# Performance work log

Measured on AMD Instinct MI355X. Metric: run time of the kernel, lower is better.

## Reference

```python
import jax, jax.numpy as jnp
import numpy as np

M, B, C = 8, 65536, 100  # model_num, batch_size, choice_size


def setup_inputs() -> dict:
    key = jax.random.key(0)
    k1, k2, k3, k4, k5, k6 = jax.random.split(key, 6)
    x = jax.random.normal(k1, (B, C), dtype=jnp.float32)
    z = jax.random.normal(k2, (M, B, C), dtype=jnp.float32)
    # choice index per customer; value == C means "no purchase" -> all-zero row
    choice = jax.random.randint(k3, (B,), 0, C + 1)
    y = (jnp.arange(C)[None, :] == choice[:, None]).astype(jnp.float32)
    alpha = jax.random.uniform(k4, (M,), dtype=jnp.float32)
    alpha = alpha / alpha.sum()  # mixture weights
    u_previous = jax.random.normal(k5, (M,), dtype=jnp.float32)
    u = jax.random.normal(k6, (), dtype=jnp.float32)
    return {"x": x, "y": y, "z": z, "alpha": alpha,
            "u_previous": u_previous, "u": u}


def reference(x, y, z, alpha, u_previous, u):
    u = jnp.reshape(u, ())
    has_y = jnp.sum(y, axis=-1) > 0                       # [B] purchased?
    # --- mixture term g (per customer), detached like torch's float(g) ---
    zy = jnp.einsum('mbc,bc->mb', z, y)                   # sum(z[j,i]*y[i])
    exp_up = jnp.exp(u_previous)[:, None]                 # [M,1]
    denom_z = exp_up + jnp.sum(jnp.exp(z), axis=-1)       # [M,B]
    num_z = jnp.where(has_y[None, :], jnp.exp(zy), exp_up)
    g = jnp.sum(alpha[:, None] * num_z / denom_z, axis=0)  # [B]
    g = jax.lax.stop_gradient(g)                          # float(g) in torch
    # --- outer model likelihood ratio ---
    xy = jnp.sum(x * y, axis=-1)                          # [B]
    denom_x = jnp.exp(u) + jnp.sum(jnp.exp(x), axis=-1)   # [B]
    num_x = jnp.where(has_y, jnp.exp(xy), jnp.exp(u))     # [B]
    loss = jnp.mean(num_x / (denom_x * g))
    return -loss
```

## Files before the change

### kernel.cpp

```cpp
#include <hip/hip_runtime.h>


constexpr int Mn = 8;
constexpr int Bn = 65536;
constexpr int Cn = 100;

__global__ __launch_bounds__(256, 4) void mmnl_kernel(
    const float* __restrict__ x,
    const float* __restrict__ y,
    const float* __restrict__ z,
    const float* __restrict__ alpha,
    const float* __restrict__ u_previous,
    const float* __restrict__ u_scalar,
    float* __restrict__ out)
{
    const int lane = threadIdx.x & 63;
    const int wib  = threadIdx.x >> 6;
    const int wid  = blockIdx.x * 4 + wib;
    const int nw   = gridDim.x * 4;

    const float exp_u = __expf(u_scalar[0]);
    float a_m[Mn], eup[Mn];
    #pragma unroll
    for (int m = 0; m < Mn; ++m) {
        a_m[m] = alpha[m];
        eup[m] = __expf(u_previous[m]);
    }

    const int  c0  = lane;
    const int  c1  = lane + 64;
    const bool hc1 = (c1 < Cn);

    float acc = 0.0f;

    for (int b = wid; b < Bn; b += nw) {
        const float* xb = x + (size_t)b * Cn;
        const float* yb = y + (size_t)b * Cn;
        float xv0 = xb[c0];
        float yv0 = yb[c0];
        float xv1 = hc1 ? xb[c1] : 0.0f;
        float yv1 = hc1 ? yb[c1] : 0.0f;

        float zv0[Mn], zv1[Mn];
        #pragma unroll
        for (int m = 0; m < Mn; ++m) {
            const float* zr = z + ((size_t)m * Bn + b) * (size_t)Cn;
            zv0[m] = zr[c0];
            zv1[m] = hc1 ? zr[c1] : 0.0f;
        }

        unsigned long long b0 = __ballot(yv0 > 0.5f);
        unsigned long long b1 = __ballot(yv1 > 0.5f);
        const bool has_y = (b0 | b1) != 0ULL;
        int  src  = 0;
        bool use1 = false;
        if (b0)       { src = __ffsll(b0) - 1; }
        else if (b1)  { src = __ffsll(b1) - 1; use1 = true; }

        float sex = __expf(xv0) + (hc1 ? __expf(xv1) : 0.0f);
        #pragma unroll
        for (int off = 32; off; off >>= 1)
            sex += __shfl_xor(sex, off, 64);

        float xy = __shfl(use1 ? xv1 : xv0, src, 64);

        float g = 0.0f;
        #pragma unroll
        for (int m = 0; m < Mn; ++m) {
            float sez = __expf(zv0[m]) + (hc1 ? __expf(zv1[m]) : 0.0f);
            #pragma unroll
            for (int off = 32; off; off >>= 1)
                sez += __shfl_xor(sez, off, 64);
            float zy  = __shfl(use1 ? zv1[m] : zv0[m], src, 64);
            float num = has_y ? __expf(zy) : eup[m];
            g += a_m[m] * num / (eup[m] + sez);
        }

        const float denom_x = exp_u + sex;
        const float num_x   = has_y ? __expf(xy) : exp_u;
        acc += num_x / (denom_x * g);
    }

    __shared__ float bsum[4];
    if (lane == 0) bsum[wib] = acc;
    __syncthreads();
    if (threadIdx.x == 0) {
        float s = (bsum[0] + bsum[1]) + (bsum[2] + bsum[3]);
        atomicAdd(out, -s * (1.0f / (float)Bn));
    }
}

extern "C" void kernel_launch(void* const* d_in, const int* in_sizes, int n_in,
                              void* d_out, int out_size, void* d_ws, size_t ws_size,
                              hipStream_t stream) {
    const float* x  = (const float*)d_in[0];
    const float* y  = (const float*)d_in[1];
    const float* z  = (const float*)d_in[2];
    const float* al = (const float*)d_in[3];
    const float* up = (const float*)d_in[4];
    const float* u  = (const float*)d_in[5];

    float* out = (float*)d_out;
    hipMemsetAsync(out, 0, sizeof(float), stream);

    dim3 grid(2048), block(256);
    mmnl_kernel<<<grid, block, 0, stream>>>(x, y, z, al, up, u, out);
}
```

Before: 336.7 us.

## Use float4 loads with two rows per wave and a two-stage reduction

Each wave now handles two batch rows, one per 32-lane half, and 25 lanes load each row with float4 vector loads instead of scalar loads spread over two 64-lane passes. The grid is sized so every wave handles exactly one row pair, with no grid-stride loop. The memset and atomicAdd are replaced by per-block partial sums written to the workspace and a second single-block reduction kernel. Divisions become hardware reciprocals. The aim is to raise memory throughput on this bandwidth-bound kernel (about 2 GB of z), at the cost of a second launch, lower reciprocal precision, and 7 of every 32 lanes sitting idle.

```diff
diff --git a/kernel.cpp b/kernel.cpp
--- a/kernel.cpp
+++ b/kernel.cpp
@@ -4,90 +4,106 @@
 constexpr int Mn = 8;
 constexpr int Bn = 65536;
 constexpr int Cn = 100;
+constexpr int NBLK = 8192;
 
-__global__ __launch_bounds__(256, 4) void mmnl_kernel(
+__device__ __forceinline__ float sel4(float4 v, int j) {
+    float r = (j == 1) ? v.y : v.x;
+    r = (j == 2) ? v.z : r;
+    r = (j == 3) ? v.w : r;
+    return r;
+}
+
+__global__ __launch_bounds__(256) void mmnl_main(
     const float* __restrict__ x,
     const float* __restrict__ y,
     const float* __restrict__ z,
     const float* __restrict__ alpha,
-    const float* __restrict__ u_previous,
-    const float* __restrict__ u_scalar,
-    float* __restrict__ out)
+    const float* __restrict__ up,
+    const float* __restrict__ us,
+    float* __restrict__ part)
 {
     const int lane = threadIdx.x & 63;
+    const int half = lane >> 5;
+    const int hl   = lane & 31;
     const int wib  = threadIdx.x >> 6;
     const int wid  = blockIdx.x * 4 + wib;
-    const int nw   = gridDim.x * 4;
+    const bool act = (hl < 25);
 
-    const float exp_u = __expf(u_scalar[0]);
-    float a_m[Mn], eup[Mn];
+    const float exp_u = __expf(us[0]);
+
+    const int    b    = wid * 2 + half;
+    const size_t roff = (size_t)b * Cn + hl * 4;
+
+    float4 xv = make_float4(0.f, 0.f, 0.f, 0.f);
+    float4 yv = xv;
+    float4 zv[Mn];
+    #pragma unroll
+    for (int m = 0; m < Mn; ++m) zv[m] = xv;
+    if (act) {
+        xv = *(const float4*)(x + roff);
+        yv = *(const float4*)(y + roff);
+        #pragma unroll
+        for (int m = 0; m < Mn; ++m)
+            zv[m] = *(const float4*)(z + (size_t)m * ((size_t)Bn * Cn) + roff);
+    }
+
+    int loc = (yv.x > 0.5f) ? 0 : -1;
+    loc = (yv.y > 0.5f) ? 1 : loc;
+    loc = (yv.z > 0.5f) ? 2 : loc;
+    loc = (yv.w > 0.5f) ? 3 : loc;
+    const unsigned long long bal = __ballot(loc >= 0);
+    const unsigned hb = (unsigned)(bal >> (half * 32));
+    const bool has_y = (hb != 0u);
+    const int  src   = has_y ? (__ffs(hb) - 1) : 0;
+    const int  srclane = half * 32 + src;
+    const int  j = __shfl(loc, srclane, 64);
+
+    float pex = __expf(xv.x) + __expf(xv.y) + __expf(xv.z) + __expf(xv.w);
+    pex = act ? pex : 0.f;
+    #pragma unroll
+    for (int off = 1; off <= 16; off <<= 1) pex += __shfl_xor(pex, off, 64);
+    const float xy = __shfl(sel4(xv, j), srclane, 64);
+
+    float g = 0.f;
     #pragma unroll
     for (int m = 0; m < Mn; ++m) {
-        a_m[m] = alpha[m];
-        eup[m] = __expf(u_previous[m]);
+        float pez = __expf(zv[m].x) + __expf(zv[m].y) +
+                    __expf(zv[m].z) + __expf(zv[m].w);
+        pez = act ? pez : 0.f;
+        #pragma unroll
+        for (int off = 1; off <= 16; off <<= 1) pez += __shfl_xor(pez, off, 64);
+        const float zc  = __shfl(sel4(zv[m], j), srclane, 64);
+        const float e   = __expf(up[m]);
+        const float num = has_y ? __expf(zc) : e;
+        g += (alpha[m] * num) * __builtin_amdgcn_rcpf(e + pez);
     }
 
-    const int  c0  = lane;
-    const int  c1  = lane + 64;
-    const bool hc1 = (c1 < Cn);
+    const float denom_x = exp_u + pex;
+    const float num_x   = has_y ? __expf(xy) : exp_u;
+    const float r       = num_x * __builtin_amdgcn_rcpf(denom_x * g);
 
-    float acc = 0.0f;
+    const float tot = r + __shfl_xor(r, 32, 64);
 
-    for (int b = wid; b < Bn; b += nw) {
-        const float* xb = x + (size_t)b * Cn;
-        const float* yb = y + (size_t)b * Cn;
-        float xv0 = xb[c0];
-        float yv0 = yb[c0];
-        float xv1 = hc1 ? xb[c1] : 0.0f;
-        float yv1 = hc1 ? yb[c1] : 0.0f;
+    __shared__ float ls[4];
+    if (lane == 0) ls[wib] = tot;
+    __syncthreads();
+    if (threadIdx.x == 0)
+        part[blockIdx.x] = (ls[0] + ls[1]) + (ls[2] + ls[3]);
+}
 
-        float zv0[Mn], zv1[Mn];
-        #pragma unroll
-        for (int m = 0; m < Mn; ++m) {
-            const float* zr = z + ((size_t)m * Bn + b) * (size_t)Cn;
-            zv0[m] = zr[c0];
-            zv1[m] = hc1 ? zr[c1] : 0.0f;
-        }
-
-        unsigned long long b0 = __ballot(yv0 > 0.5f);
-        unsigned long long b1 = __ballot(yv1 > 0.5f);
-        const bool has_y = (b0 | b1) != 0ULL;
-        int  src  = 0;
-        bool use1 = false;
-        if (b0)       { src = __ffsll(b0) - 1; }
-        else if (b1)  { src = __ffsll(b1) - 1; use1 = true; }
-
-        float sex = __expf(xv0) + (hc1 ? __expf(xv1) : 0.0f);
-        #pragma unroll
-        for (int off = 32; off; off >>= 1)
-            sex += __shfl_xor(sex, off, 64);
-
-        float xy = __shfl(use1 ? xv1 : xv0, src, 64);
-
-        float g = 0.0f;
-        #pragma unroll
-        for (int m = 0; m < Mn; ++m) {
-            float sez = __expf(zv0[m]) + (hc1 ? __expf(zv1[m]) : 0.0f);
-            #pragma unroll
-            for (int off = 32; off; off >>= 1)
-                sez += __shfl_xor(sez, off, 64);
-            float zy  = __shfl(use1 ? zv1[m] : zv0[m], src, 64);
-            float num = has_y ? __expf(zy) : eup[m];
-            g += a_m[m] * num / (eup[m] + sez);
-        }
-
-        const float denom_x = exp_u + sex;
-        const float num_x   = has_y ? __expf(xy) : exp_u;
-        acc += num_x / (denom_x * g);
-    }
-
-    __shared__ float bsum[4];
-    if (lane == 0) bsum[wib] = acc;
+__global__ __launch_bounds__(256) void mmnl_reduce(
+    const float* __restrict__ part, float* __restrict__ out)
+{
+    float s = 0.f;
+    for (int i = threadIdx.x; i < NBLK; i += 256) s += part[i];
+    #pragma unroll
+    for (int off = 1; off <= 32; off <<= 1) s += __shfl_xor(s, off, 64);
+    __shared__ float ls[4];
+    const int wib = threadIdx.x >> 6;
+    if ((threadIdx.x & 63) == 0) ls[wib] = s;
     __syncthreads();
-    if (threadIdx.x == 0) {
-        float s = (bsum[0] + bsum[1]) + (bsum[2] + bsum[3]);
-        atomicAdd(out, -s * (1.0f / (float)Bn));
-    }
+    if (threadIdx.x == 0)
+        out[0] = -((ls[0] + ls[1]) + (ls[2] + ls[3])) * (1.0f / (float)Bn);
 }
 
 extern "C" void kernel_launch(void* const* d_in, const int* in_sizes, int n_in,
@@ -100,9 +116,9 @@
     const float* up = (const float*)d_in[4];
     const float* u  = (const float*)d_in[5];
 
-    float* out = (float*)d_out;
-    hipMemsetAsync(out, 0, sizeof(float), stream);
+    float* part = (float*)d_ws;
+    float* out  = (float*)d_out;
 
-    dim3 grid(2048), block(256);
-    mmnl_kernel<<<grid, block, 0, stream>>>(x, y, z, al, up, u, out);
+    mmnl_main<<<dim3(NBLK), dim3(256), 0, stream>>>(x, y, z, al, up, u, part);
+    mmnl_reduce<<<dim3(1), dim3(256), 0, stream>>>(part, out);
 }
```

Measured after the change: 333.1 us. No clear change (-1.0%).
